# Optimization experiments

Hardware: AMD Instinct MI355X
Metric: run time of the kernel (lower is better)

Reference implementation:

```python
import jax, jax.numpy as jnp
import numpy as np

DIM = 1024
HEADS = 16
HD = DIM // HEADS          # 64
SPECIAL = 8                # CLS/register tokens with full attention
GRID = 32                  # 32x32 patch grid
N = SPECIAL + GRID * GRID  # 1032
B = 8
WINDOW = 3                 # 2D sliding-window radius (7x7 box)
EPS = 1e-6


def _make_2d_mask() -> jnp.ndarray:
    """[N, N] bool mask: special tokens attend everywhere; patches use 2D local box."""
    idx = np.arange(N)
    special = (idx[:, None] < SPECIAL) | (idx[None, :] < SPECIAL)
    p = idx - SPECIAL
    r, c = p // GRID, p % GRID
    swa = (np.abs(r[:, None] - r[None, :]) <= WINDOW) & (np.abs(c[:, None] - c[None, :]) <= WINDOW)
    return jnp.asarray(special | swa)

_MASK = _make_2d_mask()


def setup_inputs() -> dict:
    key = jax.random.key(0)
    k1, k2, k3 = jax.random.split(key, 3)
    hidden_states = jax.random.normal(k1, (B, N, DIM), dtype=jnp.float32)
    qkv_w = jax.random.normal(k2, (3 * DIM, DIM), dtype=jnp.float32) * 0.02
    out_w = jax.random.normal(k3, (DIM, DIM), dtype=jnp.float32) * 0.02
    norm_q_w = jnp.ones((HD,), dtype=jnp.float32)
    norm_k_w = jnp.ones((HD,), dtype=jnp.float32)
    # Standard RoPE tables, half-dim frequencies tiled twice (rotate-half convention)
    pos = np.arange(N, dtype=np.float32)
    inv_freq = 1.0 / (10000.0 ** (np.arange(0, HD, 2, dtype=np.float32) / HD))
    ang = pos[:, None] * inv_freq[None, :]              # [N, HD/2]
    freqs_cos = jnp.asarray(np.concatenate([np.cos(ang), np.cos(ang)], axis=-1))  # [N, HD]
    freqs_sin = jnp.asarray(np.concatenate([np.sin(ang), np.sin(ang)], axis=-1))
    return dict(hidden_states=hidden_states, freqs_cos=freqs_cos, freqs_sin=freqs_sin,
                qkv_w=qkv_w, out_w=out_w, norm_q_w=norm_q_w, norm_k_w=norm_k_w)


def _rms_norm(x, w):
    return x * jax.lax.rsqrt(jnp.mean(x * x, axis=-1, keepdims=True) + EPS) * w


def _rotate_half(x):
    return jnp.concatenate([-x[..., HD // 2:], x[..., :HD // 2]], axis=-1)


def reference(hidden_states, freqs_cos, freqs_sin, qkv_w, out_w, norm_q_w, norm_k_w):
    Bn, Nn, C = hidden_states.shape
    # Fused QKV projection -> [3, B, H, N, D]
    qkv = (hidden_states @ qkv_w.T).reshape(Bn, Nn, 3, HEADS, HD).transpose(2, 0, 3, 1, 4)
    q, k, v = qkv[0], qkv[1], qkv[2]
    # per-head-dim RMSNorm on q, k
    q = _rms_norm(q, norm_q_w)
    k = _rms_norm(k, norm_k_w)
    # RoPE
    cos = freqs_cos[None, None]  # [1,1,N,D]
    sin = freqs_sin[None, None]
    q = q * cos + _rotate_half(q) * sin
    k = k * cos + _rotate_half(k) * sin
    # 2D sliding-window + global-token masked attention
    scale = 1.0 / jnp.sqrt(jnp.asarray(HD, dtype=q.dtype))
    scores = jnp.einsum('bhqd,bhkd->bhqk', q, k) * scale
    neg = jnp.asarray(jnp.finfo(scores.dtype).min, scores.dtype)
    scores = jnp.where(_MASK[None, None], scores, neg)
    probs = jax.nn.softmax(scores, axis=-1)
    attn = jnp.einsum('bhqk,bhkd->bhqd', probs, v)
    attn = attn.transpose(0, 2, 1, 3).reshape(Bn, Nn, C)
    return attn @ out_w.T
```

## Files before the change

kernel.cpp:

```cpp
#include <hip/hip_runtime.h>
#include <hip/hip_bf16.h>

typedef unsigned short ushort_t;
typedef __bf16 bf16x8 __attribute__((ext_vector_type(8)));
typedef float f32x4 __attribute__((ext_vector_type(4)));
typedef float f32x8 __attribute__((ext_vector_type(8)));

#define NTOK 1032
#define NROWS 8256
#define DIMC 1024
#define QKV_ELEMS 8454144
#define XE 8454144
#define QWE 3145728
#define OWE 1048576

__device__ __forceinline__ float bf2f(ushort_t u) {
    union { unsigned int i; float f; } v; v.i = ((unsigned int)u) << 16; return v.f;
}
__device__ __forceinline__ ushort_t f2bf(float f) {
    union { float f; unsigned int i; } v; v.f = f;
    unsigned int r = v.i + 0x7fffu + ((v.i >> 16) & 1u);
    return (ushort_t)(r >> 16);
}
__device__ __forceinline__ bf16x8 cvt8(const float* p) {
    const float4 a = *(const float4*)p;
    const float4 b = *(const float4*)(p + 4);
    bf16x8 r;
    r[0] = (__bf16)a.x; r[1] = (__bf16)a.y; r[2] = (__bf16)a.z; r[3] = (__bf16)a.w;
    r[4] = (__bf16)b.x; r[5] = (__bf16)b.y; r[6] = (__bf16)b.z; r[7] = (__bf16)b.w;
    return r;
}
__device__ __forceinline__ void load_lds16(const ushort_t* g, ushort_t* l) {
    __builtin_amdgcn_global_load_lds(
        (const __attribute__((address_space(1))) unsigned int*)g,
        (__attribute__((address_space(3))) unsigned int*)l, 16, 0, 0);
}

__global__ __launch_bounds__(256) void cvt_kernel(
    const float* __restrict__ X, const float* __restrict__ Wq,
    const float* __restrict__ Wo,
    ushort_t* __restrict__ Xb, ushort_t* __restrict__ Wqb,
    ushort_t* __restrict__ Wob)
{
    const long i8 = ((long)blockIdx.x * 256 + threadIdx.x) * 8;
    const float* src;
    ushort_t* dst;
    long off;
    if (i8 < XE)            { src = X;  dst = Xb;  off = i8; }
    else if (i8 < XE + QWE) { src = Wq; dst = Wqb; off = i8 - XE; }
    else                    { src = Wo; dst = Wob; off = i8 - XE - QWE; }
    *(bf16x8*)(dst + off) = cvt8(src + off);
}

template<int MODE>
__global__ __launch_bounds__(512, 2) void gemm256_kernel(
    const ushort_t* __restrict__ A, const ushort_t* __restrict__ W,
    ushort_t* __restrict__ QKV, float* __restrict__ Out,
    const float* __restrict__ cosb, const float* __restrict__ sinb,
    const float* __restrict__ nqw, const float* __restrict__ nkw)
{
    constexpr int SMEM_BYTES = (MODE == 0) ? 135168 : 131072;
    __shared__ __align__(16) unsigned char SMEM[SMEM_BYTES];
    ushort_t* A_lds = (ushort_t*)SMEM;
    ushort_t* B_lds = (ushort_t*)(SMEM + 65536);

    const int tid  = threadIdx.x;
    const int wave = tid >> 6, lane = tid & 63;
    const int wr = wave >> 2, wc = wave & 3;
    const int fr = lane & 15, quad = lane >> 4;
    const int m0 = blockIdx.y * 256;
    const int n0 = blockIdx.x * 256;
    const bool swap = (MODE == 1) || (blockIdx.x < 8);

    int aoff[4], boff[4];
    #pragma unroll
    for (int ld = 0; ld < 4; ++ld) {
        const int s   = ld * 512 + tid;
        const int row = s >> 3;
        const int kc  = ((s & 7) ^ (row & 7)) * 8;
        int ar = m0 + row; if (ar > NROWS - 1) ar = NROWS - 1;
        aoff[ld] = ar * DIMC + kc;
        boff[ld] = (n0 + row) * DIMC + kc;
    }

    const int ck0 = (quad ^ (fr & 7)) * 8;
    const int ck1 = ((quad + 4) ^ (fr & 7)) * 8;
    const int abase = (wr * 128 + fr) * 64;
    const int bbase = (wc * 64 + fr) * 64;

    f32x4 acc[8][4] = {};

#define SA(ld, t, c) load_lds16(A + aoff[ld] + (t) * 64, \
                                &A_lds[(c) * 16384 + ((ld) * 512 + tid) * 8])
#define SB(ld, t, c) load_lds16(W + boff[ld] + (t) * 64, \
                                &B_lds[(c) * 16384 + ((ld) * 512 + tid) * 8])
#define WAIT_LGKM0 asm volatile("s_waitcnt lgkmcnt(0)" ::: "memory")
#define WAIT_VM6   asm volatile("s_waitcnt vmcnt(6)"  ::: "memory")
#define WAIT_VM0   asm volatile("s_waitcnt vmcnt(0)"  ::: "memory")

#define READ_AF(p) \
    af[0][0] = *(const bf16x8*)&A_lds[cb + abase + ((p) * 2 + 0) * 1024 + ck0]; \
    af[0][1] = *(const bf16x8*)&A_lds[cb + abase + ((p) * 2 + 0) * 1024 + ck1]; \
    af[1][0] = *(const bf16x8*)&A_lds[cb + abase + ((p) * 2 + 1) * 1024 + ck0]; \
    af[1][1] = *(const bf16x8*)&A_lds[cb + abase + ((p) * 2 + 1) * 1024 + ck1];

#define MFMA_PHASE(p) \
    __builtin_amdgcn_s_setprio(1); \
    if (swap) { \
        _Pragma("unroll") \
        for (int mfi = 0; mfi < 2; ++mfi) \
            _Pragma("unroll") \
            for (int nf = 0; nf < 4; ++nf) { \
                acc[(p) * 2 + mfi][nf] = __builtin_amdgcn_mfma_f32_16x16x32_bf16( \
                    bfrag[nf][0], af[mfi][0], acc[(p) * 2 + mfi][nf], 0, 0, 0); \
                acc[(p) * 2 + mfi][nf] = __builtin_amdgcn_mfma_f32_16x16x32_bf16( \
                    bfrag[nf][1], af[mfi][1], acc[(p) * 2 + mfi][nf], 0, 0, 0); \
            } \
    } else { \
        _Pragma("unroll") \
        for (int mfi = 0; mfi < 2; ++mfi) \
            _Pragma("unroll") \
            for (int nf = 0; nf < 4; ++nf) { \
                acc[(p) * 2 + mfi][nf] = __builtin_amdgcn_mfma_f32_16x16x32_bf16( \
                    af[mfi][0], bfrag[nf][0], acc[(p) * 2 + mfi][nf], 0, 0, 0); \
                acc[(p) * 2 + mfi][nf] = __builtin_amdgcn_mfma_f32_16x16x32_bf16( \
                    af[mfi][1], bfrag[nf][1], acc[(p) * 2 + mfi][nf], 0, 0, 0); \
            } \
    } \
    __builtin_amdgcn_s_setprio(0);

    SB(0, 0, 0); SB(1, 0, 0); SB(2, 0, 0); SB(3, 0, 0);
    SA(0, 0, 0); SA(1, 0, 0); SA(2, 0, 0); SA(3, 0, 0);
    SB(0, 1, 1); SB(1, 1, 1); SB(2, 1, 1); SB(3, 1, 1);
    SA(0, 1, 1); SA(2, 1, 1);
    WAIT_VM6;
    __builtin_amdgcn_s_barrier();

    for (int t = 0; t < 16; ++t) {
        const int c = t & 1, o = c ^ 1;
        const int cb = c * 16384;
        bf16x8 bfrag[4][2];
        bf16x8 af[2][2];

        #pragma unroll
        for (int nf = 0; nf < 4; ++nf) {
            bfrag[nf][0] = *(const bf16x8*)&B_lds[cb + bbase + nf * 1024 + ck0];
            bfrag[nf][1] = *(const bf16x8*)&B_lds[cb + bbase + nf * 1024 + ck1];
        }
        READ_AF(0);
        if (t < 15) { SA(1, t + 1, o); SA(3, t + 1, o); }
        __builtin_amdgcn_s_barrier();
        WAIT_LGKM0; __builtin_amdgcn_sched_barrier(0);
        MFMA_PHASE(0);
        __builtin_amdgcn_s_barrier();

        READ_AF(1);
        if (t < 14) { SB(0, t + 2, c); SB(1, t + 2, c);
                      SB(2, t + 2, c); SB(3, t + 2, c); }
        __builtin_amdgcn_s_barrier();
        WAIT_LGKM0; __builtin_amdgcn_sched_barrier(0);
        MFMA_PHASE(1);
        __builtin_amdgcn_s_barrier();

        READ_AF(2);
        if (t < 14) { SA(0, t + 2, c); SA(2, t + 2, c); }
        __builtin_amdgcn_s_barrier();
        WAIT_LGKM0; __builtin_amdgcn_sched_barrier(0);
        MFMA_PHASE(2);

        READ_AF(3);
        __builtin_amdgcn_s_barrier();
        WAIT_LGKM0; __builtin_amdgcn_sched_barrier(0);
        MFMA_PHASE(3);

        if (t < 14)       { WAIT_VM6; __builtin_amdgcn_s_barrier(); }
        else if (t == 14) { WAIT_VM0; __builtin_amdgcn_s_barrier(); }
    }

    const int rb = quad * 4;
    if (MODE == 1) {
        #pragma unroll
        for (int mf = 0; mf < 8; ++mf) {
            const int m = m0 + wr * 128 + mf * 16 + fr;
            if (m < NROWS) {
                #pragma unroll
                for (int nf = 0; nf < 4; ++nf) {
                    const int o_ = n0 + wc * 64 + nf * 16 + rb;
                    float4 pk;
                    pk.x = acc[mf][nf][0];
                    pk.y = acc[mf][nf][1];
                    pk.z = acc[mf][nf][2];
                    pk.w = acc[mf][nf][3];
                    *(float4*)(Out + (long)m * DIMC + o_) = pk;
                }
            }
        }
    } else if (swap) {
        const int part   = n0 >> 10;
        const int hgbase = ((n0 & 1023) + wc * 64) >> 6;
        const float* wtab = (part == 0) ? nqw : nkw;

        float* T = (float*)SMEM;
        __syncthreads();
        for (int e = tid; e < 256 * 16; e += 512) {
            const int row = e >> 4, seg = e & 15;
            const int mm  = m0 + row;
            const int bb2 = mm / NTOK;
            const int n2  = mm - bb2 * NTOK;
            const float4 c4 = *(const float4*)(cosb + n2 * 64 + seg * 4);
            const float4 s4 = *(const float4*)(sinb + n2 * 64 + seg * 4);
            const float4 wf = *(const float4*)(wtab + seg * 4);
            const float4 wp = *(const float4*)(wtab + ((seg ^ 8) * 4));
            float* dst = T + row * 132 + seg * 8;
            ((float2*)dst)[0] = make_float2(c4.x * wf.x, s4.x * wp.x);
            ((float2*)dst)[1] = make_float2(c4.y * wf.y, s4.y * wp.y);
            ((float2*)dst)[2] = make_float2(c4.z * wf.z, s4.z * wp.z);
            ((float2*)dst)[3] = make_float2(c4.w * wf.w, s4.w * wp.w);
        }
        __syncthreads();

#define QK_NF(MF, NF, PN, SGN) { \
        const float4 q0 = *(const float4*)(trow + ((NF) * 16 + rb) * 2); \
        const float4 q1 = *(const float4*)(trow + ((NF) * 16 + rb) * 2 + 4); \
        ushort4 pk; \
        pk.x = f2bf(rms * (acc[MF][NF][0] * q0.x + (SGN) * acc[MF][PN][0] * q0.y)); \
        pk.y = f2bf(rms * (acc[MF][NF][1] * q0.z + (SGN) * acc[MF][PN][1] * q0.w)); \
        pk.z = f2bf(rms * (acc[MF][NF][2] * q1.x + (SGN) * acc[MF][PN][2] * q1.y)); \
        pk.w = f2bf(rms * (acc[MF][NF][3] * q1.z + (SGN) * acc[MF][PN][3] * q1.w)); \
        *(ushort4*)(outb + (NF) * 16) = pk; }

#define QK_MF(MF) { \
        const int rr = wr * 128 + (MF) * 16 + fr; \
        const int m  = m0 + rr; \
        if (m < NROWS) { \
            const int bb = m / NTOK, n = m - bb * NTOK; \
            float ss = 0.f; \
            _Pragma("unroll") \
            for (int nf = 0; nf < 4; ++nf) { \
                ss += acc[MF][nf][0] * acc[MF][nf][0]; \
                ss += acc[MF][nf][1] * acc[MF][nf][1]; \
                ss += acc[MF][nf][2] * acc[MF][nf][2]; \
                ss += acc[MF][nf][3] * acc[MF][nf][3]; \
            } \
            ss += __shfl_xor(ss, 16, 64); \
            ss += __shfl_xor(ss, 32, 64); \
            const float rms = rsqrtf(ss * (1.0f / 64.0f) + 1e-6f); \
            const float* trow = T + rr * 132; \
            ushort_t* outb = QKV + (long)part * QKV_ELEMS + \
                ((long)(bb * 16 + hgbase) * NTOK + n) * 64 + rb; \
            QK_NF(MF, 0, 2, -1.f) \
            QK_NF(MF, 1, 3, -1.f) \
            QK_NF(MF, 2, 0,  1.f) \
            QK_NF(MF, 3, 1,  1.f) \
        } }

        QK_MF(0) QK_MF(1) QK_MF(2) QK_MF(3)
        QK_MF(4) QK_MF(5) QK_MF(6) QK_MF(7)
#undef QK_MF
#undef QK_NF
    } else {
        const int hg = ((n0 & 1023) + wc * 64) >> 6;
        #pragma unroll
        for (int nf = 0; nf < 4; ++nf) {
            const int d = nf * 16 + fr;
            #pragma unroll
            for (int mf = 0; mf < 8; ++mf) {
                const int mb = m0 + wr * 128 + mf * 16 + rb;
                if (mb < NROWS) {
                    const int bb = mb / NTOK, n = mb - bb * NTOK;
                    ushort4 pk;
                    pk.x = f2bf(acc[mf][nf][0]);
                    pk.y = f2bf(acc[mf][nf][1]);
                    pk.z = f2bf(acc[mf][nf][2]);
                    pk.w = f2bf(acc[mf][nf][3]);
                    *(ushort4*)(QKV + 2L * QKV_ELEMS +
                        ((long)((bb * 16 + hg) * 64 + d)) * NTOK + n) = pk;
                }
            }
        }
    }
#undef SA
#undef SB
#undef WAIT_LGKM0
#undef WAIT_VM6
#undef WAIT_VM0
#undef READ_AF
#undef MFMA_PHASE
}

__global__ __launch_bounds__(256) void attn_kernel(
    const ushort_t* __restrict__ Qb, const ushort_t* __restrict__ Kb,
    const ushort_t* __restrict__ Vt, ushort_t* __restrict__ AO)
{
    __shared__ __align__(16) ushort_t KP_s[256 * 72];

    const int tid = threadIdx.x;
    const int wave = tid >> 6, lane = tid & 63;
    const int m_ = lane & 15, quad = lane >> 4;
    const int nb = wave * 64;
    const int d0 = wave * 16;

    bf16x8 ones;
    #pragma unroll
    for (int e = 0; e < 8; ++e) ones[e] = (__bf16)1.0f;

    if (blockIdx.x >= 128) {
        const int blk = blockIdx.x - 128;
        const int bh = blk & 127, qr = blk >> 7;
        const int b = bh >> 4, h = bh & 15;

        int r0 = qr - 3; if (r0 < 0) r0 = 0;
        int r1 = qr + 3; if (r1 > 31) r1 = 31;
        const int limit = 8 + (r1 - r0 + 1) * 32;

        const ushort_t* Qg  = Qb + ((long)bh * NTOK + 8 + qr * 32) * 64;
        const ushort_t* Kg  = Kb + (long)bh * NTOK * 64;
        const ushort_t* Vtg = Vt + (long)bh * 64 * NTOK;

        bf16x8 af[2][2];
        #pragma unroll
        for (int mt = 0; mt < 2; ++mt)
            #pragma unroll
            for (int ks = 0; ks < 2; ++ks)
                af[mt][ks] = *(const bf16x8*)(Qg + (mt * 16 + m_) * 64 + ks * 32 + quad * 8);

        bf16x8 bv[8];
        #pragma unroll
        for (int ks = 0; ks < 8; ++ks) {
            const int slot0 = ks * 32 + quad * 8;
            int tok0;
            if (slot0 >= limit) tok0 = 0;
            else if (slot0 < 8) tok0 = slot0;
            else tok0 = 8 + r0 * 32 + (slot0 - 8);
            bv[ks] = *(const bf16x8*)(Vtg + (long)(d0 + m_) * NTOK + tok0);
        }

        for (int c = tid; c < limit * 8; c += 256) {
            const int slot = c >> 3, c8 = (c & 7) * 8;
            const int tok = slot + (slot >= 8 ? r0 * 32 : 0);
            *(bf16x8*)&KP_s[slot * 72 + c8] = *(const bf16x8*)(Kg + (long)tok * 64 + c8);
        }
        __syncthreads();

        bf16x8 bfr[4][2];
        #pragma unroll
        for (int nt = 0; nt < 4; ++nt)
            #pragma unroll
            for (int ks = 0; ks < 2; ++ks)
                bfr[nt][ks] = *(const bf16x8*)&KP_s[(nb + nt * 16 + m_) * 72 + ks * 32 + quad * 8];

        f32x4 sacc[2][4] = {};
        #pragma unroll
        for (int mt = 0; mt < 2; ++mt)
            #pragma unroll
            for (int nt = 0; nt < 4; ++nt) {
                sacc[mt][nt] = __builtin_amdgcn_mfma_f32_16x16x32_bf16(
                    af[mt][0], bfr[nt][0], sacc[mt][nt], 0, 0, 0);
                sacc[mt][nt] = __builtin_amdgcn_mfma_f32_16x16x32_bf16(
                    af[mt][1], bfr[nt][1], sacc[mt][nt], 0, 0, 0);
            }
        __syncthreads();

        #pragma unroll
        for (int mt = 0; mt < 2; ++mt)
            #pragma unroll
            for (int nt = 0; nt < 4; ++nt) {
                const int slot = nb + nt * 16 + m_;
                const int kc = (slot - 8) & 31;
                #pragma unroll
                for (int reg = 0; reg < 4; ++reg) {
                    const int qm = mt * 16 + quad * 4 + reg;
                    const bool val = (slot < 8) ||
                        ((slot < limit) && ((unsigned)(kc - qm + 3) <= 6u));
                    const float p = val ? __expf(sacc[mt][nt][reg] * 0.125f) : 0.f;
                    KP_s[qm * 280 + slot] = f2bf(p);
                }
            }
        __syncthreads();

        f32x4 oacc[2] = {}, lacc[2] = {};
        #pragma unroll
        for (int ks = 0; ks < 8; ++ks) {
            #pragma unroll
            for (int mt = 0; mt < 2; ++mt) {
                const bf16x8 ap = *(const bf16x8*)&KP_s[(mt * 16 + m_) * 280 + ks * 32 + quad * 8];
                oacc[mt] = __builtin_amdgcn_mfma_f32_16x16x32_bf16(ap, bv[ks], oacc[mt], 0, 0, 0);
                lacc[mt] = __builtin_amdgcn_mfma_f32_16x16x32_bf16(ap, ones,   lacc[mt], 0, 0, 0);
            }
        }
        #pragma unroll
        for (int mt = 0; mt < 2; ++mt)
            #pragma unroll
            for (int reg = 0; reg < 4; ++reg) {
                const int qm = mt * 16 + quad * 4 + reg;
                const int tok = 8 + qr * 32 + qm;
                AO[((long)(b * NTOK + tok)) * DIMC + h * 64 + d0 + m_] =
                    f2bf(oacc[mt][reg] / lacc[mt][reg]);
            }
    } else {
        const int bh = blockIdx.x;
        const int b = bh >> 4, h = bh & 15;
        const ushort_t* Kg  = Kb + (long)bh * NTOK * 64;
        const ushort_t* Vtg = Vt + (long)bh * 64 * NTOK;

        bf16x8 afs[2];
        if (m_ < 8) {
            #pragma unroll
            for (int ks = 0; ks < 2; ++ks)
                afs[ks] = *(const bf16x8*)(Qb + ((long)bh * NTOK + m_) * 64 + ks * 32 + quad * 8);
        } else {
            #pragma unroll
            for (int ks = 0; ks < 2; ++ks)
                #pragma unroll
                for (int e = 0; e < 8; ++e) afs[ks][e] = (__bf16)0.f;
        }

        f32x4 oacc = {}, lacc = {};
        for (int ch = 0; ch < 5; ++ch) {
            const int tok0 = ch * 256;
            const int limit = (NTOK - tok0 < 256) ? (NTOK - tok0) : 256;

            bf16x8 bv[8];
            #pragma unroll
            for (int ks = 0; ks < 8; ++ks) {
                const int slot0 = ks * 32 + quad * 8;
                const int tok = tok0 + ((slot0 < limit) ? slot0 : 0);
                bv[ks] = *(const bf16x8*)(Vtg + (long)(d0 + m_) * NTOK + tok);
            }

            __syncthreads();
            for (int c = tid; c < limit * 8; c += 256) {
                const int slot = c >> 3, c8 = (c & 7) * 8;
                *(bf16x8*)&KP_s[slot * 72 + c8] =
                    *(const bf16x8*)(Kg + (long)(tok0 + slot) * 64 + c8);
            }
            __syncthreads();

            bf16x8 bfr[4][2];
            #pragma unroll
            for (int nt = 0; nt < 4; ++nt)
                #pragma unroll
                for (int ks = 0; ks < 2; ++ks)
                    bfr[nt][ks] = *(const bf16x8*)&KP_s[(nb + nt * 16 + m_) * 72 + ks * 32 + quad * 8];
            f32x4 sacc[4] = {};
            #pragma unroll
            for (int nt = 0; nt < 4; ++nt) {
                sacc[nt] = __builtin_amdgcn_mfma_f32_16x16x32_bf16(afs[0], bfr[nt][0], sacc[nt], 0, 0, 0);
                sacc[nt] = __builtin_amdgcn_mfma_f32_16x16x32_bf16(afs[1], bfr[nt][1], sacc[nt], 0, 0, 0);
            }
            __syncthreads();

            #pragma unroll
            for (int nt = 0; nt < 4; ++nt) {
                const int slot = nb + nt * 16 + m_;
                const bool val = (slot < limit);
                #pragma unroll
                for (int reg = 0; reg < 4; ++reg) {
                    const int qm = quad * 4 + reg;
                    const float p = val ? __expf(sacc[nt][reg] * 0.125f) : 0.f;
                    KP_s[qm * 280 + slot] = f2bf(p);
                }
            }
            __syncthreads();

            #pragma unroll
            for (int ks = 0; ks < 8; ++ks) {
                const bf16x8 ap = *(const bf16x8*)&KP_s[m_ * 280 + ks * 32 + quad * 8];
                oacc = __builtin_amdgcn_mfma_f32_16x16x32_bf16(ap, bv[ks], oacc, 0, 0, 0);
                lacc = __builtin_amdgcn_mfma_f32_16x16x32_bf16(ap, ones,   lacc, 0, 0, 0);
            }
        }

        #pragma unroll
        for (int reg = 0; reg < 4; ++reg) {
            const int qm = quad * 4 + reg;
            if (qm < 8) {
                AO[((long)(b * NTOK + qm)) * DIMC + h * 64 + d0 + m_] =
                    f2bf(oacc[reg] / lacc[reg]);
            }
        }
    }
}

extern "C" void kernel_launch(void* const* d_in, const int* in_sizes, int n_in,
                              void* d_out, int out_size, void* d_ws, size_t ws_size,
                              hipStream_t stream) {
    const float* X    = (const float*)d_in[0];
    const float* fc   = (const float*)d_in[1];
    const float* fs   = (const float*)d_in[2];
    const float* qkvw = (const float*)d_in[3];
    const float* outw = (const float*)d_in[4];
    const float* nqw  = (const float*)d_in[5];
    const float* nkw  = (const float*)d_in[6];

    ushort_t* Qb  = (ushort_t*)d_ws;
    ushort_t* Kb  = Qb + QKV_ELEMS;
    ushort_t* Vt  = Kb + QKV_ELEMS;
    ushort_t* AO  = Vt + QKV_ELEMS;
    ushort_t* Xb  = AO + QKV_ELEMS;
    ushort_t* Wqb = Xb + XE;
    ushort_t* Wob = Wqb + QWE;
    float* Out = (float*)d_out;

    cvt_kernel<<<6176, 256, 0, stream>>>(X, qkvw, outw, Xb, Wqb, Wob);
    gemm256_kernel<0><<<dim3(12, 33), 512, 0, stream>>>(Xb, Wqb, Qb, nullptr,
                                                        fc, fs, nqw, nkw);
    attn_kernel<<<4224, 256, 0, stream>>>(Qb, Kb, Vt, AO);
    gemm256_kernel<1><<<dim3(4, 33), 512, 0, stream>>>(AO, Wob, nullptr, Out,
                                                       fc, fs, nqw, nkw);
}
```

Before: 254.9 us.

## Load K fragments directly from global and remap GEMM workgroups across XCDs

The attention kernel now reads K operand fragments straight from global memory into registers instead of staging them through LDS. This removes the cooperative copy and two barriers per chunk, and lets the LDS buffer shrink to the probability tile only. Separately, the GEMM kernel remaps its linear block id so that consecutive tiles land on the same XCD, which is meant to improve L2 reuse. The cost is more scattered, uncoalesced global loads for K.

```diff
diff --git a/kernel.cpp b/kernel.cpp
--- a/kernel.cpp
+++ b/kernel.cpp
@@ -64,13 +64,24 @@
     ushort_t* A_lds = (ushort_t*)SMEM;
     ushort_t* B_lds = (ushort_t*)(SMEM + 65536);
 
+    constexpr int GX  = (MODE == 0) ? 12 : 4;
+    constexpr int NWG = GX * 33;
+    constexpr int QW  = NWG >> 3, RW = NWG & 7;
+    {
+    }
+    const int orig = blockIdx.y * GX + blockIdx.x;
+    const int xcd  = orig & 7, li = orig >> 3;
+    const int wgid = (xcd < RW ? xcd * (QW + 1)
+                               : RW * (QW + 1) + (xcd - RW) * QW) + li;
+    const int bx = wgid % GX, by = wgid / GX;
+
     const int tid  = threadIdx.x;
     const int wave = tid >> 6, lane = tid & 63;
     const int wr = wave >> 2, wc = wave & 3;
     const int fr = lane & 15, quad = lane >> 4;
-    const int m0 = blockIdx.y * 256;
-    const int n0 = blockIdx.x * 256;
-    const bool swap = (MODE == 1) || (blockIdx.x < 8);
+    const int m0 = by * 256;
+    const int n0 = bx * 256;
+    const bool swap = (MODE == 1) || (bx < 8);
 
     int aoff[4], boff[4];
     #pragma unroll
@@ -292,7 +303,7 @@
     const ushort_t* __restrict__ Qb, const ushort_t* __restrict__ Kb,
     const ushort_t* __restrict__ Vt, ushort_t* __restrict__ AO)
 {
-    __shared__ __align__(16) ushort_t KP_s[256 * 72];
+    __shared__ __align__(16) ushort_t KP_s[32 * 280];
 
     const int tid = threadIdx.x;
     const int wave = tid >> 6, lane = tid & 63;
@@ -335,19 +346,16 @@
             bv[ks] = *(const bf16x8*)(Vtg + (long)(d0 + m_) * NTOK + tok0);
         }
 
-        for (int c = tid; c < limit * 8; c += 256) {
-            const int slot = c >> 3, c8 = (c & 7) * 8;
-            const int tok = slot + (slot >= 8 ? r0 * 32 : 0);
-            *(bf16x8*)&KP_s[slot * 72 + c8] = *(const bf16x8*)(Kg + (long)tok * 64 + c8);
-        }
-        __syncthreads();
-
         bf16x8 bfr[4][2];
         #pragma unroll
-        for (int nt = 0; nt < 4; ++nt)
+        for (int nt = 0; nt < 4; ++nt) {
+            const int slot = nb + nt * 16 + m_;
+            int tok = (slot < 8) ? slot : (slot + r0 * 32);
+            if (slot >= limit) tok = 0;
             #pragma unroll
             for (int ks = 0; ks < 2; ++ks)
-                bfr[nt][ks] = *(const bf16x8*)&KP_s[(nb + nt * 16 + m_) * 72 + ks * 32 + quad * 8];
+                bfr[nt][ks] = *(const bf16x8*)(Kg + (long)tok * 64 + ks * 32 + quad * 8);
+        }
 
         f32x4 sacc[2][4] = {};
         #pragma unroll
@@ -359,7 +367,6 @@
                 sacc[mt][nt] = __builtin_amdgcn_mfma_f32_16x16x32_bf16(
                     af[mt][1], bfr[nt][1], sacc[mt][nt], 0, 0, 0);
             }
-        __syncthreads();
 
         #pragma unroll
         for (int mt = 0; mt < 2; ++mt)
@@ -428,28 +435,23 @@
                 bv[ks] = *(const bf16x8*)(Vtg + (long)(d0 + m_) * NTOK + tok);
             }
 
-            __syncthreads();
-            for (int c = tid; c < limit * 8; c += 256) {
-                const int slot = c >> 3, c8 = (c & 7) * 8;
-                *(bf16x8*)&KP_s[slot * 72 + c8] =
-                    *(const bf16x8*)(Kg + (long)(tok0 + slot) * 64 + c8);
-            }
-            __syncthreads();
-
             bf16x8 bfr[4][2];
             #pragma unroll
-            for (int nt = 0; nt < 4; ++nt)
+            for (int nt = 0; nt < 4; ++nt) {
+                const int slot = nb + nt * 16 + m_;
+                const int tok = tok0 + ((slot < limit) ? slot : 0);
                 #pragma unroll
                 for (int ks = 0; ks < 2; ++ks)
-                    bfr[nt][ks] = *(const bf16x8*)&KP_s[(nb + nt * 16 + m_) * 72 + ks * 32 + quad * 8];
+                    bfr[nt][ks] = *(const bf16x8*)(Kg + (long)tok * 64 + ks * 32 + quad * 8);
+            }
             f32x4 sacc[4] = {};
             #pragma unroll
             for (int nt = 0; nt < 4; ++nt) {
                 sacc[nt] = __builtin_amdgcn_mfma_f32_16x16x32_bf16(afs[0], bfr[nt][0], sacc[nt], 0, 0, 0);
                 sacc[nt] = __builtin_amdgcn_mfma_f32_16x16x32_bf16(afs[1], bfr[nt][1], sacc[nt], 0, 0, 0);
             }
+
             __syncthreads();
-
             #pragma unroll
             for (int nt = 0; nt < 4; ++nt) {
                 const int slot = nb + nt * 16 + m_;
```

New measurement: 249.7 us. -2.0%, faster.
